# Kernel tuning notes

Hardware: AMD Instinct MI355X
Metric: run time of the kernel (lower is better)

Reference implementation:

```python
import jax, jax.numpy as jnp
import numpy as np

B, S, H = 4, 2048, 1024
DECAY_RATE = 0.5  # MemoryModule decay: exp(-decay_rate * k), k=1 (most recent pattern)


def setup_inputs() -> dict:
    key = jax.random.key(0)
    ks = jax.random.split(key, 7)
    hidden_states = jax.random.normal(ks[0], (B, S, H), dtype=jnp.float32)
    # past attention pattern: valid row-stochastic attention probs [B, S, S]
    pa = jax.random.uniform(ks[1], (B, S, S), dtype=jnp.float32)
    past_attention = pa / pa.sum(-1, keepdims=True)
    scale = 1.0 / np.sqrt(H).astype(np.float32)
    Wq = jax.random.normal(ks[2], (H, H), dtype=jnp.float32) * scale
    Wk = jax.random.normal(ks[3], (H, H), dtype=jnp.float32) * scale
    Wv = jax.random.normal(ks[4], (H, H), dtype=jnp.float32) * scale
    Wm = jax.random.normal(ks[5], (H, H), dtype=jnp.float32) * scale
    w_gate = jax.random.normal(ks[6], (H,), dtype=jnp.float32) * scale
    return {"hidden_states": hidden_states, "past_attention": past_attention,
            "Wq": Wq, "Wk": Wk, "Wv": Wv, "Wm": Wm, "w_gate": w_gate}


def reference(hidden_states, past_attention, Wq, Wk, Wv, Wm, w_gate):
    h = hidden_states.shape[-1]
    inv_sqrt_h = 1.0 / (h ** 0.5)
    # QKV projections (hidden -> hidden)
    q = jnp.einsum('bsh,hd->bsd', hidden_states, Wq)
    k = jnp.einsum('bsh,hd->bsd', hidden_states, Wk)
    v = jnp.einsum('bsh,hd->bsd', hidden_states, Wv)
    # base attention scores QK^T / sqrt(H)
    scores = jnp.einsum('bqd,bkd->bqk', q, k) * inv_sqrt_h
    # --- memory bias ---
    # decayed history pattern (single most-recent entry, k=1)
    memory = past_attention * jnp.exp(jnp.float32(-DECAY_RATE * 1.0))  # [B,S,S]
    # per-token scalar gate from query
    gates = jax.nn.sigmoid(jnp.einsum('bsh,h->bs', q, w_gate))  # [B,S]
    memory_values = jnp.einsum('bqk,bkd->bqd', memory, v)        # memory @ V
    transformed = jnp.einsum('bsh,hd->bsd', memory_values, Wm)   # memory_transform (no bias)
    gated_memory = gates[..., None] * transformed
    memory_bias = jnp.einsum('bqd,bkd->bqk', gated_memory, k) * inv_sqrt_h
    # augmented attention
    probs = jax.nn.softmax(scores + memory_bias, axis=-1)
    context = jnp.einsum('bqk,bkd->bqd', probs, v)
    return context
```

## Files before the change

kernel.cpp:

```cpp
#include <hip/hip_runtime.h>
#include <hip/hip_bf16.h>

typedef __attribute__((ext_vector_type(4))) float f32x4;
typedef __attribute__((ext_vector_type(8))) __bf16 bf16x8;

__device__ __forceinline__ unsigned short f2bf(float f) {
    union { float f; unsigned u; } x; x.f = f;
    unsigned r = x.u + 0x7fffu + ((x.u >> 16) & 1u);
    return (unsigned short)(r >> 16);
}
__device__ __forceinline__ float bf2f(unsigned short b) {
    union { unsigned u; float f; } x; x.u = ((unsigned)b) << 16;
    return x.f;
}

__device__ __forceinline__ void gload16(const void* g, void* l) {
    __builtin_amdgcn_global_load_lds(
        (const __attribute__((address_space(1))) unsigned int*)g,
        (__attribute__((address_space(3))) unsigned int*)l,
        16, 0, 0);
}

template <int N> __device__ __forceinline__ void vm_wait();
template <> __device__ __forceinline__ void vm_wait<0>() { asm volatile("s_waitcnt vmcnt(0)" ::: "memory"); }
template <> __device__ __forceinline__ void vm_wait<2>() { asm volatile("s_waitcnt vmcnt(2)" ::: "memory"); }
template <> __device__ __forceinline__ void vm_wait<4>() { asm volatile("s_waitcnt vmcnt(4)" ::: "memory"); }

__global__ __launch_bounds__(256) void k_prep(
    const float* __restrict__ hs, const float* __restrict__ pa,
    const float* __restrict__ Wq, const float* __restrict__ Wk,
    const float* __restrict__ Wv, const float* __restrict__ Wm,
    unsigned short* __restrict__ hs_bf, unsigned short* __restrict__ pa_bf,
    unsigned short* __restrict__ WT, float decay) {
    __shared__ float tile[32][33];
    unsigned b = blockIdx.x;
    int t = threadIdx.x;
    if (b < 16384u) {
        int i = b * 256 + t;
        float4 v = reinterpret_cast<const float4*>(pa)[i];
        union { unsigned short u[4]; uint2 q; } o;
        o.u[0] = f2bf(v.x * decay); o.u[1] = f2bf(v.y * decay);
        o.u[2] = f2bf(v.z * decay); o.u[3] = f2bf(v.w * decay);
        reinterpret_cast<uint2*>(pa_bf)[i] = o.q;
    } else if (b < 24576u) {
        int i = (b - 16384u) * 256 + t;
        float4 v = reinterpret_cast<const float4*>(hs)[i];
        union { unsigned short u[4]; uint2 q; } o;
        o.u[0] = f2bf(v.x); o.u[1] = f2bf(v.y);
        o.u[2] = f2bf(v.z); o.u[3] = f2bf(v.w);
        reinterpret_cast<uint2*>(hs_bf)[i] = o.q;
    } else {
        unsigned bb = b - 24576u;
        int z = bb >> 10, rem = bb & 1023;
        int bx = rem & 31, by = rem >> 5;
        const float* src = z == 0 ? Wq : z == 1 ? Wk : z == 2 ? Wv : Wm;
        unsigned short* dst = WT + (size_t)z * 1024 * 1024;
        int lx = t & 31, ly8 = t >> 5;
        int x = bx * 32 + lx;
#pragma unroll
        for (int i = 0; i < 4; i++)
            tile[ly8 + i * 8][lx] = src[(size_t)(by * 32 + ly8 + i * 8) * 1024 + x];
        __syncthreads();
        int tx = by * 32 + lx;
#pragma unroll
        for (int i = 0; i < 4; i++)
            dst[(size_t)(bx * 32 + ly8 + i * 8) * 1024 + tx] = f2bf(tile[lx][ly8 + i * 8]);
    }
}

__global__ __launch_bounds__(256) void k_post(
    const unsigned short* __restrict__ C3, unsigned short* __restrict__ v_t,
    const float* __restrict__ wg, float* __restrict__ gates) {
    __shared__ unsigned short tile[32][33];
    unsigned b = blockIdx.x;
    int t = threadIdx.x;
    if (b < 8192u) {
        int bx = b & 31, by = (b >> 5) & 63, bz = b >> 11;
        int lx = t & 31, ly8 = t >> 5;
        int x = bx * 32 + lx;
#pragma unroll
        for (int i = 0; i < 4; i++) {
            int y = by * 32 + ly8 + i * 8;
            tile[ly8 + i * 8][lx] = C3[(size_t)(bz * 2048 + y) * 3072 + 2048 + x];
        }
        __syncthreads();
        int tx = by * 32 + lx;
#pragma unroll
        for (int i = 0; i < 4; i++) {
            int ty = bx * 32 + ly8 + i * 8;
            v_t[(size_t)bz * 1024 * 2048 + (size_t)ty * 2048 + tx] = tile[lx][ly8 + i * 8];
        }
    } else {
        unsigned bb = b - 8192u;
        int lane = t & 63;
        int row = bb * 4 + (t >> 6);
        const unsigned short* qr = C3 + (size_t)row * 3072 + lane * 16;
        uint4 a0 = *reinterpret_cast<const uint4*>(qr);
        uint4 a1 = *reinterpret_cast<const uint4*>(qr + 8);
        const float* wp = wg + lane * 16;
        float s = 0.f;
        unsigned ua[8] = {a0.x, a0.y, a0.z, a0.w, a1.x, a1.y, a1.z, a1.w};
#pragma unroll
        for (int j = 0; j < 8; j++) {
            s += bf2f((unsigned short)(ua[j] & 0xffff)) * wp[2 * j];
            s += bf2f((unsigned short)(ua[j] >> 16)) * wp[2 * j + 1];
        }
#pragma unroll
        for (int o = 1; o < 64; o <<= 1) s += __shfl_xor(s, o);
        if (lane == 0) gates[row] = 1.f / (1.f + __expf(-s));
    }
}

__global__ __launch_bounds__(256) void k_inv(const float* __restrict__ partials,
                                             float* __restrict__ inv_s) {
    int r = blockIdx.x * 256 + threadIdx.x;
    const float4* p = reinterpret_cast<const float4*>(partials + (size_t)r * 8);
    float4 a = p[0], b = p[1];
    inv_s[r] = 1.f / (a.x + a.y + a.z + a.w + b.x + b.y + b.z + b.w);
}

template <int BN>
struct Geo {
    static constexpr int WN = BN / 64;
    static constexpr int WM = 8 / WN;
    static constexpr int WROWS = 256 / WM;
    static constexpr int MF = WROWS / 16;
    static constexpr int MP = MF / 4;
    static constexpr int ASZ = 256 * 64 * 2;
    static constexpr int BSZ = BN * 64 * 2;
    static constexpr int BUFSZ = ASZ + BSZ;
};

#define GPH(BUFOFF, MB, LB, STG, VMW)                                                   \
    {                                                                                   \
        const char* aB = smem + (BUFOFF);                                               \
        const char* bB = aB + G::ASZ;                                                   \
        bf16x8 af[G::MP * 2];                                                           \
        _Pragma("unroll") for (int mm = 0; mm < G::MP; ++mm)                            \
        _Pragma("unroll") for (int kk = 0; kk < 2; ++kk) {                              \
            int rowx = wrow + ((MB) + mm) * 16 + fr;                                    \
            int slot = (kk * 4 + kq) ^ (rowx & 7);                                      \
            af[mm * 2 + kk] = *reinterpret_cast<const bf16x8*>(aB + rowx * 128 + slot * 16); \
        }                                                                               \
        if (LB) {                                                                       \
            _Pragma("unroll") for (int nn = 0; nn < 4; ++nn)                            \
            _Pragma("unroll") for (int kk = 0; kk < 2; ++kk) {                          \
                int rowx = wcol + nn * 16 + fr;                                         \
                int slot = (kk * 4 + kq) ^ (rowx & 7);                                  \
                bfrag[nn * 2 + kk] = *reinterpret_cast<const bf16x8*>(bB + rowx * 128 + slot * 16); \
            }                                                                           \
        }                                                                               \
        STG;                                                                            \
        __builtin_amdgcn_sched_barrier(0);                                              \
        VMW;                                                                            \
        __builtin_amdgcn_s_barrier();                                                   \
        asm volatile("s_waitcnt lgkmcnt(0)" ::: "memory");                              \
        __builtin_amdgcn_sched_barrier(0);                                              \
        __builtin_amdgcn_s_setprio(1);                                                  \
        _Pragma("unroll") for (int mm = 0; mm < G::MP; ++mm)                            \
        _Pragma("unroll") for (int nn = 0; nn < 4; ++nn)                                \
        _Pragma("unroll") for (int kk = 0; kk < 2; ++kk)                                \
            acc[(MB) + mm][nn] = __builtin_amdgcn_mfma_f32_16x16x32_bf16(               \
                af[mm * 2 + kk], bfrag[nn * 2 + kk], acc[(MB) + mm][nn], 0, 0, 0);      \
        __builtin_amdgcn_s_setprio(0);                                                  \
        __builtin_amdgcn_sched_barrier(0);                                              \
        __builtin_amdgcn_s_barrier();                                                   \
        __builtin_amdgcn_sched_barrier(0);                                              \
    }

template <int EPI, int BN>
__global__ __launch_bounds__(512, 2) void k_gemm8(
    const unsigned short* __restrict__ A, int ldA, long long bsA,
    const unsigned short* __restrict__ Bt, int ldB, long long bsB,
    void* __restrict__ Cv, int ldC, long long bsC,
    const unsigned short* __restrict__ Qm, int ldQ,
    const float* __restrict__ gates, float alpha, int K,
    int NX, int NY, int NB, int yf) {
    using G = Geo<BN>;
    extern __shared__ char smem[];
    const int NT = K >> 6, NI = K >> 7;

    unsigned b = blockIdx.x;
    unsigned wg = (b & 7) * (gridDim.x >> 3) + (b >> 3);
    int xT, yT, zB;
    if (yf) {
        yT = wg % NY; unsigned r2 = wg / NY;
        xT = r2 % NX; zB = (int)(r2 / NX) % NB;
    } else {
        xT = wg % NX; unsigned r2 = wg / NX;
        yT = r2 % NY; zB = (int)(r2 / NY) % NB;
    }

    const unsigned short* Ab = A + (size_t)zB * (size_t)bsA;
    const unsigned short* Bb = Bt + (size_t)zB * (size_t)bsB;

    int t = threadIdx.x, lane = t & 63, wave = t >> 6;
    int wc = wave % G::WN, wr = wave / G::WN;
    int fr = lane & 15, kq = lane >> 4;
    int wrow = wr * G::WROWS, wcol = wc * 64;
    int trow = t >> 3, csx = (t & 7) ^ (trow & 7);
    long long rowTile = (long long)yT * 256, colTile = (long long)xT * BN;

    f32x4 acc[G::MF][4];
#pragma unroll
    for (int m = 0; m < G::MF; ++m)
#pragma unroll
        for (int n = 0; n < 4; ++n) acc[m][n] = (f32x4){0.f, 0.f, 0.f, 0.f};
    bf16x8 bfrag[8];

    auto stageA = [&](int buf, int h, int tt) {
        int kt = tt < NT ? tt : NT - 1;
#pragma unroll
        for (int rr = 0; rr < 2; ++rr) {
            const unsigned short* src =
                Ab + (size_t)(rowTile + h * 128 + rr * 64 + trow) * (size_t)ldA + kt * 64 + csx * 8;
            gload16(src, smem + buf * G::BUFSZ + h * 16384 + rr * 8192 + t * 16);
        }
    };
    auto stageB = [&](int buf, int h, int tt) {
        int kt = tt < NT ? tt : NT - 1;
        if (BN == 256) {
#pragma unroll
            for (int rr = 0; rr < 2; ++rr) {
                const unsigned short* src =
                    Bb + (size_t)(colTile + h * 128 + rr * 64 + trow) * (size_t)ldB + kt * 64 + csx * 8;
                gload16(src, smem + buf * G::BUFSZ + G::ASZ + h * 16384 + rr * 8192 + t * 16);
            }
        } else {
            const unsigned short* src =
                Bb + (size_t)(colTile + h * 64 + trow) * (size_t)ldB + kt * 64 + csx * 8;
            gload16(src, smem + buf * G::BUFSZ + G::ASZ + h * 8192 + t * 16);
        }
    };

    stageA(0, 0, 0); stageA(0, 1, 0);
    stageB(0, 0, 0); stageB(0, 1, 0);
    stageB(1, 0, 1); stageB(1, 1, 1);
    __builtin_amdgcn_sched_barrier(0);
    vm_wait<0>();
    __builtin_amdgcn_s_barrier();
    __builtin_amdgcn_sched_barrier(0);

    constexpr int VMN = (BN == 256) ? 4 : 2;
    for (int i = 0; i < NI; ++i) {
        int t1 = 2 * i + 1, t2 = 2 * i + 2, t3 = 2 * i + 3;
        GPH(0,          0,         1, stageA(1, 0, t1), (void)0);
        GPH(0,          G::MP,     0, stageA(1, 1, t1), (void)0);
        GPH(0,          2 * G::MP, 0, stageB(0, 0, t2), (void)0);
        GPH(0,          3 * G::MP, 0, stageB(0, 1, t2), vm_wait<VMN>());
        GPH(G::BUFSZ,   0,         1, stageA(0, 0, t2), (void)0);
        GPH(G::BUFSZ,   G::MP,     0, stageA(0, 1, t2), (void)0);
        GPH(G::BUFSZ,   2 * G::MP, 0, stageB(1, 0, t3), (void)0);
        GPH(G::BUFSZ,   3 * G::MP, 0, stageB(1, 1, t3), vm_wait<VMN>());
    }
    vm_wait<0>();

    long long rb0 = rowTile + wrow + kq * 4;
    long long cb0 = colTile + wcol + fr;
    if (EPI == 0) {
        unsigned short* C = (unsigned short*)Cv + (size_t)zB * (size_t)bsC;
#pragma unroll
        for (int m = 0; m < G::MF; ++m)
#pragma unroll
            for (int n = 0; n < 4; ++n)
#pragma unroll
                for (int r = 0; r < 4; ++r)
                    C[(size_t)(rb0 + m * 16 + r) * (size_t)ldC + cb0 + n * 16] =
                        f2bf(acc[m][n][r] * alpha);
    } else if (EPI == 1) {
        unsigned short* C = (unsigned short*)Cv;
#pragma unroll
        for (int m = 0; m < G::MF; ++m)
#pragma unroll
            for (int r = 0; r < 4; ++r) {
                long long row = rb0 + m * 16 + r;
                float g = gates[row];
#pragma unroll
                for (int n = 0; n < 4; ++n) {
                    long long col = cb0 + n * 16;
                    float v = (bf2f(Qm[(size_t)row * (size_t)ldQ + col]) + g * acc[m][n][r]) * alpha;
                    C[(size_t)row * (size_t)ldC + col] = f2bf(v);
                }
            }
    } else if (EPI == 4) {
        float* C = (float*)Cv + (size_t)zB * (size_t)bsC;
#pragma unroll
        for (int m = 0; m < G::MF; ++m)
#pragma unroll
            for (int r = 0; r < 4; ++r) {
                long long row = rb0 + m * 16 + r;
                float g = gates[(size_t)zB * (size_t)ldQ + row];
#pragma unroll
                for (int n = 0; n < 4; ++n)
                    C[(size_t)row * (size_t)ldC + cb0 + n * 16] = acc[m][n][r] * g;
            }
    } else if (EPI == 5) {
        unsigned short* C = (unsigned short*)Cv + (size_t)zB * (size_t)bsC;
        float* partials = (float*)gates;
        float srow[G::MF][4];
#pragma unroll
        for (int m = 0; m < G::MF; ++m)
#pragma unroll
            for (int r = 0; r < 4; ++r) srow[m][r] = 0.f;
#pragma unroll
        for (int m = 0; m < G::MF; ++m)
#pragma unroll
            for (int n = 0; n < 4; ++n)
#pragma unroll
                for (int r = 0; r < 4; ++r) {
                    float e = __expf(acc[m][n][r] * alpha);
                    C[(size_t)(rb0 + m * 16 + r) * (size_t)ldC + cb0 + n * 16] = f2bf(e);
                    srow[m][r] += e;
                }
#pragma unroll
        for (int m = 0; m < G::MF; ++m)
#pragma unroll
            for (int r = 0; r < 4; ++r) {
#pragma unroll
                for (int msk = 1; msk < 16; msk <<= 1)
                    srow[m][r] += __shfl_xor(srow[m][r], msk);
            }
        float* sums = (float*)smem;
        if (fr == 0) {
#pragma unroll
            for (int m = 0; m < G::MF; ++m)
#pragma unroll
                for (int r = 0; r < 4; ++r)
                    sums[(wrow + kq * 4 + m * 16 + r) * G::WN + wc] = srow[m][r];
        }
        __syncthreads();
        if (t < 256) {
            float s = 0.f;
#pragma unroll
            for (int j = 0; j < G::WN; ++j) s += sums[t * G::WN + j];
            partials[((size_t)zB * 2048 + (size_t)rowTile + t) * 8 + xT] = s;
        }
    }
}

extern "C" void kernel_launch(void* const* d_in, const int* in_sizes, int n_in,
                              void* d_out, int out_size, void* d_ws, size_t ws_size,
                              hipStream_t stream) {
    const float* hs = (const float*)d_in[0];
    const float* pa = (const float*)d_in[1];
    const float* Wq = (const float*)d_in[2];
    const float* Wk = (const float*)d_in[3];
    const float* Wv = (const float*)d_in[4];
    const float* Wm = (const float*)d_in[5];
    const float* wg = (const float*)d_in[6];
    float* out = (float*)d_out;

    const int B = 4, S = 2048, H = 1024;
    const size_t BS = (size_t)B * S;
    const size_t BSH = BS * H;
    const size_t BSS = (size_t)B * S * S;
    const float inv_sqrt_h = 0.03125f;
    const float decay = 0.60653065971263342f;

    char* ws = (char*)d_ws;
    size_t off = 0;
    auto take = [&](size_t bytes) {
        char* p = ws + off;
        off += (bytes + 255) & ~(size_t)255;
        return p;
    };
    unsigned short* hs_bf = (unsigned short*)take(BSH * 2);
    unsigned short* WT    = (unsigned short*)take(4ull * H * H * 2);
    float* gates          = (float*)take(BS * 4);
    unsigned short* C3    = (unsigned short*)take(BS * 3 * H * 2);
    unsigned short* v_t   = (unsigned short*)take(BSH * 2);
    unsigned short* pa_bf = (unsigned short*)take(BSS * 2);
    float* partials       = (float*)take(BS * 8 * 4);
    float* inv_s          = (float*)take(BS * 4);
    unsigned short* mv    = (unsigned short*)d_out;
    unsigned short* u_bf  = hs_bf;
    unsigned short* probs = pa_bf;
    unsigned short* WmT   = WT + 3ull * H * H;

    (void)hipFuncSetAttribute((const void*)k_gemm8<0, 128>, hipFuncAttributeMaxDynamicSharedMemorySize, 98304);
    (void)hipFuncSetAttribute((const void*)k_gemm8<1, 128>, hipFuncAttributeMaxDynamicSharedMemorySize, 98304);
    (void)hipFuncSetAttribute((const void*)k_gemm8<4, 128>, hipFuncAttributeMaxDynamicSharedMemorySize, 98304);
    (void)hipFuncSetAttribute((const void*)k_gemm8<5, 256>, hipFuncAttributeMaxDynamicSharedMemorySize, 131072);

    k_prep<<<dim3(28672), 256, 0, stream>>>(hs, pa, Wq, Wk, Wv, Wm, hs_bf, pa_bf, WT, decay);
    k_gemm8<0, 128><<<768, 512, 98304, stream>>>(
        hs_bf, H, 0, WT, H, 0, C3, 3 * H, 0, nullptr, 0, nullptr, 1.f, H, 24, 32, 1, 0);
    k_post<<<dim3(10240), 256, 0, stream>>>(C3, v_t, wg, gates);
    k_gemm8<0, 128><<<256, 512, 98304, stream>>>(
        pa_bf, S, (long long)S * S, v_t, S, (long long)H * S, mv, H, (long long)S * H,
        nullptr, 0, nullptr, 1.f, S, 8, 8, 4, 1);
    k_gemm8<1, 128><<<256, 512, 98304, stream>>>(
        mv, H, 0, WmT, H, 0, u_bf, H, 0, C3, 3 * H, gates, inv_sqrt_h, H, 8, 32, 1, 0);
    k_gemm8<5, 256><<<256, 512, 131072, stream>>>(
        u_bf, H, (long long)S * H, C3 + H, 3 * H, (long long)S * 3 * H,
        probs, S, (long long)S * S, nullptr, 0, partials, 1.f, H, 8, 8, 4, 1);
    k_inv<<<dim3(32), 256, 0, stream>>>(partials, inv_s);
    k_gemm8<4, 128><<<256, 512, 98304, stream>>>(
        probs, S, (long long)S * S, v_t, S, (long long)H * S, out, H, (long long)S * H,
        nullptr, S, inv_s, 1.f, S, 8, 8, 4, 1);
}
```

Baseline: 251.4 us.

## Fold gate projection into Wq·w_gate, fuse softmax normalization into ctx epilogue

Precomputes wg2 = Wq·w_gate so each token's gate becomes a dot product of hidden_states with wg2, evaluated in fp32 inside the hs conversion pass rather than as a separate read of the bf16 q. The k_inv launch goes away because the ctx GEMM epilogue now sums the 8 partial row sums and inverts them itself. The GEMM template is also split into distinctly named kernels, and the qkv and u launches switch their yf raster flag to 1. This cuts kernel launches and memory passes at the cost of a small extra kernel and redundant reciprocal work per epilogue row.

Result: slower. 259.0 us (+3.0%).

```diff
diff --git a/kernel.cpp b/kernel.cpp
--- a/kernel.cpp
+++ b/kernel.cpp
@@ -26,13 +26,32 @@
 template <> __device__ __forceinline__ void vm_wait<2>() { asm volatile("s_waitcnt vmcnt(2)" ::: "memory"); }
 template <> __device__ __forceinline__ void vm_wait<4>() { asm volatile("s_waitcnt vmcnt(4)" ::: "memory"); }
 
+__global__ __launch_bounds__(256) void k_wg2(const float* __restrict__ Wq,
+                                             const float* __restrict__ wg,
+                                             float* __restrict__ wg2) {
+    int lane = threadIdx.x & 63;
+    int row = blockIdx.x * 4 + (threadIdx.x >> 6);
+    const float4* a = reinterpret_cast<const float4*>(Wq + (size_t)row * 1024);
+    const float4* x = reinterpret_cast<const float4*>(wg);
+    float s = 0.f;
+    for (int i = lane; i < 256; i += 64) {
+        float4 av = a[i], bv = x[i];
+        s += av.x * bv.x + av.y * bv.y + av.z * bv.z + av.w * bv.w;
+    }
+#pragma unroll
+    for (int o = 1; o < 64; o <<= 1) s += __shfl_xor(s, o);
+    if (lane == 0) wg2[row] = s;
+}
+
 __global__ __launch_bounds__(256) void k_prep(
     const float* __restrict__ hs, const float* __restrict__ pa,
     const float* __restrict__ Wq, const float* __restrict__ Wk,
     const float* __restrict__ Wv, const float* __restrict__ Wm,
     unsigned short* __restrict__ hs_bf, unsigned short* __restrict__ pa_bf,
-    unsigned short* __restrict__ WT, float decay) {
+    unsigned short* __restrict__ WT, float decay,
+    const float* __restrict__ wg2, float* __restrict__ gates) {
     __shared__ float tile[32][33];
+    __shared__ float red[4];
     unsigned b = blockIdx.x;
     int t = threadIdx.x;
     if (b < 16384u) {
@@ -43,12 +62,23 @@
         o.u[2] = f2bf(v.z * decay); o.u[3] = f2bf(v.w * decay);
         reinterpret_cast<uint2*>(pa_bf)[i] = o.q;
     } else if (b < 24576u) {
-        int i = (b - 16384u) * 256 + t;
+        unsigned row = b - 16384u;
+        int i = row * 256 + t;
         float4 v = reinterpret_cast<const float4*>(hs)[i];
         union { unsigned short u[4]; uint2 q; } o;
         o.u[0] = f2bf(v.x); o.u[1] = f2bf(v.y);
         o.u[2] = f2bf(v.z); o.u[3] = f2bf(v.w);
         reinterpret_cast<uint2*>(hs_bf)[i] = o.q;
+        float4 w = reinterpret_cast<const float4*>(wg2)[t];
+        float s = v.x * w.x + v.y * w.y + v.z * w.z + v.w * w.w;
+#pragma unroll
+        for (int o2 = 1; o2 < 64; o2 <<= 1) s += __shfl_xor(s, o2);
+        if ((t & 63) == 0) red[t >> 6] = s;
+        __syncthreads();
+        if (t == 0) {
+            float ss = red[0] + red[1] + red[2] + red[3];
+            gates[row] = 1.f / (1.f + __expf(-ss));
+        }
     } else {
         unsigned bb = b - 24576u;
         int z = bb >> 10, rem = bb & 1023;
@@ -68,55 +98,26 @@
     }
 }
 
-__global__ __launch_bounds__(256) void k_post(
-    const unsigned short* __restrict__ C3, unsigned short* __restrict__ v_t,
-    const float* __restrict__ wg, float* __restrict__ gates) {
+__global__ __launch_bounds__(256) void k_post(const unsigned short* __restrict__ C3,
+                                              unsigned short* __restrict__ v_t) {
     __shared__ unsigned short tile[32][33];
     unsigned b = blockIdx.x;
     int t = threadIdx.x;
-    if (b < 8192u) {
-        int bx = b & 31, by = (b >> 5) & 63, bz = b >> 11;
-        int lx = t & 31, ly8 = t >> 5;
-        int x = bx * 32 + lx;
-#pragma unroll
-        for (int i = 0; i < 4; i++) {
-            int y = by * 32 + ly8 + i * 8;
-            tile[ly8 + i * 8][lx] = C3[(size_t)(bz * 2048 + y) * 3072 + 2048 + x];
-        }
-        __syncthreads();
-        int tx = by * 32 + lx;
-#pragma unroll
-        for (int i = 0; i < 4; i++) {
-            int ty = bx * 32 + ly8 + i * 8;
-            v_t[(size_t)bz * 1024 * 2048 + (size_t)ty * 2048 + tx] = tile[lx][ly8 + i * 8];
-        }
-    } else {
-        unsigned bb = b - 8192u;
-        int lane = t & 63;
-        int row = bb * 4 + (t >> 6);
-        const unsigned short* qr = C3 + (size_t)row * 3072 + lane * 16;
-        uint4 a0 = *reinterpret_cast<const uint4*>(qr);
-        uint4 a1 = *reinterpret_cast<const uint4*>(qr + 8);
-        const float* wp = wg + lane * 16;
-        float s = 0.f;
-        unsigned ua[8] = {a0.x, a0.y, a0.z, a0.w, a1.x, a1.y, a1.z, a1.w};
-#pragma unroll
-        for (int j = 0; j < 8; j++) {
-            s += bf2f((unsigned short)(ua[j] & 0xffff)) * wp[2 * j];
-            s += bf2f((unsigned short)(ua[j] >> 16)) * wp[2 * j + 1];
-        }
-#pragma unroll
-        for (int o = 1; o < 64; o <<= 1) s += __shfl_xor(s, o);
-        if (lane == 0) gates[row] = 1.f / (1.f + __expf(-s));
-    }
-}
-
-__global__ __launch_bounds__(256) void k_inv(const float* __restrict__ partials,
-                                             float* __restrict__ inv_s) {
-    int r = blockIdx.x * 256 + threadIdx.x;
-    const float4* p = reinterpret_cast<const float4*>(partials + (size_t)r * 8);
-    float4 a = p[0], b = p[1];
-    inv_s[r] = 1.f / (a.x + a.y + a.z + a.w + b.x + b.y + b.z + b.w);
+    int bx = b & 31, by = (b >> 5) & 63, bz = b >> 11;
+    int lx = t & 31, ly8 = t >> 5;
+    int x = bx * 32 + lx;
+#pragma unroll
+    for (int i = 0; i < 4; i++) {
+        int y = by * 32 + ly8 + i * 8;
+        tile[ly8 + i * 8][lx] = C3[(size_t)(bz * 2048 + y) * 3072 + 2048 + x];
+    }
+    __syncthreads();
+    int tx = by * 32 + lx;
+#pragma unroll
+    for (int i = 0; i < 4; i++) {
+        int ty = bx * 32 + ly8 + i * 8;
+        v_t[(size_t)bz * 1024 * 2048 + (size_t)ty * 2048 + tx] = tile[lx][ly8 + i * 8];
+    }
 }
 
 template <int BN>
@@ -169,7 +170,8 @@
     }
 
 template <int EPI, int BN>
-__global__ __launch_bounds__(512, 2) void k_gemm8(
+__device__ __forceinline__ void gemm_body(
+    char* smem,
     const unsigned short* __restrict__ A, int ldA, long long bsA,
     const unsigned short* __restrict__ Bt, int ldB, long long bsB,
     void* __restrict__ Cv, int ldC, long long bsC,
@@ -177,7 +179,6 @@
     const float* __restrict__ gates, float alpha, int K,
     int NX, int NY, int NB, int yf) {
     using G = Geo<BN>;
-    extern __shared__ char smem[];
     const int NT = K >> 6, NI = K >> 7;
 
     unsigned b = blockIdx.x;
@@ -289,7 +290,10 @@
 #pragma unroll
             for (int r = 0; r < 4; ++r) {
                 long long row = rb0 + m * 16 + r;
-                float g = gates[(size_t)zB * (size_t)ldQ + row];
+                const float4* pp = reinterpret_cast<const float4*>(
+                    gates + ((size_t)zB * 2048 + row) * 8);
+                float4 p0 = pp[0], p1 = pp[1];
+                float g = 1.f / (p0.x + p0.y + p0.z + p0.w + p1.x + p1.y + p1.z + p1.w);
 #pragma unroll
                 for (int n = 0; n < 4; ++n)
                     C[(size_t)row * (size_t)ldC + cb0 + n * 16] = acc[m][n][r] * g;
@@ -336,6 +340,34 @@
             partials[((size_t)zB * 2048 + (size_t)rowTile + t) * 8 + xT] = s;
         }
     }
+}
+
+#define GEMM_ARGS                                                                     \
+    const unsigned short *A, int ldA, long long bsA, const unsigned short *Bt,        \
+        int ldB, long long bsB, void *Cv, int ldC, long long bsC,                     \
+        const unsigned short *Qm, int ldQ, const float *gates, float alpha, int K,    \
+        int NX, int NY, int NB, int yf
+#define GEMM_PASS A, ldA, bsA, Bt, ldB, bsB, Cv, ldC, bsC, Qm, ldQ, gates, alpha, K, NX, NY, NB, yf
+
+__global__ __launch_bounds__(512, 2) void k_qkv(GEMM_ARGS) {
+    extern __shared__ char smem[];
+    gemm_body<0, 128>(smem, GEMM_PASS);
+}
+__global__ __launch_bounds__(512, 2) void k_mv(GEMM_ARGS) {
+    extern __shared__ char smem[];
+    gemm_body<0, 128>(smem, GEMM_PASS);
+}
+__global__ __launch_bounds__(512, 2) void k_u(GEMM_ARGS) {
+    extern __shared__ char smem[];
+    gemm_body<1, 128>(smem, GEMM_PASS);
+}
+__global__ __launch_bounds__(512, 2) void k_logits(GEMM_ARGS) {
+    extern __shared__ char smem[];
+    gemm_body<5, 256>(smem, GEMM_PASS);
+}
+__global__ __launch_bounds__(512, 2) void k_ctx(GEMM_ARGS) {
+    extern __shared__ char smem[];
+    gemm_body<4, 128>(smem, GEMM_PASS);
 }
 
 extern "C" void kernel_launch(void* const* d_in, const int* in_sizes, int n_in,
@@ -366,36 +398,37 @@
     };
     unsigned short* hs_bf = (unsigned short*)take(BSH * 2);
     unsigned short* WT    = (unsigned short*)take(4ull * H * H * 2);
+    float* wg2            = (float*)take(H * 4);
     float* gates          = (float*)take(BS * 4);
     unsigned short* C3    = (unsigned short*)take(BS * 3 * H * 2);
     unsigned short* v_t   = (unsigned short*)take(BSH * 2);
     unsigned short* pa_bf = (unsigned short*)take(BSS * 2);
     float* partials       = (float*)take(BS * 8 * 4);
-    float* inv_s          = (float*)take(BS * 4);
     unsigned short* mv    = (unsigned short*)d_out;
     unsigned short* u_bf  = hs_bf;
     unsigned short* probs = pa_bf;
     unsigned short* WmT   = WT + 3ull * H * H;
 
-    (void)hipFuncSetAttribute((const void*)k_gemm8<0, 128>, hipFuncAttributeMaxDynamicSharedMemorySize, 98304);
-    (void)hipFuncSetAttribute((const void*)k_gemm8<1, 128>, hipFuncAttributeMaxDynamicSharedMemorySize, 98304);
-    (void)hipFuncSetAttribute((const void*)k_gemm8<4, 128>, hipFuncAttributeMaxDynamicSharedMemorySize, 98304);
-    (void)hipFuncSetAttribute((const void*)k_gemm8<5, 256>, hipFuncAttributeMaxDynamicSharedMemorySize, 131072);
-
-    k_prep<<<dim3(28672), 256, 0, stream>>>(hs, pa, Wq, Wk, Wv, Wm, hs_bf, pa_bf, WT, decay);
-    k_gemm8<0, 128><<<768, 512, 98304, stream>>>(
-        hs_bf, H, 0, WT, H, 0, C3, 3 * H, 0, nullptr, 0, nullptr, 1.f, H, 24, 32, 1, 0);
-    k_post<<<dim3(10240), 256, 0, stream>>>(C3, v_t, wg, gates);
-    k_gemm8<0, 128><<<256, 512, 98304, stream>>>(
+    (void)hipFuncSetAttribute((const void*)k_qkv,    hipFuncAttributeMaxDynamicSharedMemorySize, 98304);
+    (void)hipFuncSetAttribute((const void*)k_mv,     hipFuncAttributeMaxDynamicSharedMemorySize, 98304);
+    (void)hipFuncSetAttribute((const void*)k_u,      hipFuncAttributeMaxDynamicSharedMemorySize, 98304);
+    (void)hipFuncSetAttribute((const void*)k_ctx,    hipFuncAttributeMaxDynamicSharedMemorySize, 98304);
+    (void)hipFuncSetAttribute((const void*)k_logits, hipFuncAttributeMaxDynamicSharedMemorySize, 131072);
+
+    k_wg2<<<dim3(256), 256, 0, stream>>>(Wq, wg, wg2);
+    k_prep<<<dim3(28672), 256, 0, stream>>>(hs, pa, Wq, Wk, Wv, Wm, hs_bf, pa_bf, WT, decay, wg2, gates);
+    k_qkv<<<768, 512, 98304, stream>>>(
+        hs_bf, H, 0, WT, H, 0, C3, 3 * H, 0, nullptr, 0, nullptr, 1.f, H, 24, 32, 1, 1);
+    k_post<<<dim3(8192), 256, 0, stream>>>(C3, v_t);
+    k_mv<<<256, 512, 98304, stream>>>(
         pa_bf, S, (long long)S * S, v_t, S, (long long)H * S, mv, H, (long long)S * H,
         nullptr, 0, nullptr, 1.f, S, 8, 8, 4, 1);
-    k_gemm8<1, 128><<<256, 512, 98304, stream>>>(
-        mv, H, 0, WmT, H, 0, u_bf, H, 0, C3, 3 * H, gates, inv_sqrt_h, H, 8, 32, 1, 0);
-    k_gemm8<5, 256><<<256, 512, 131072, stream>>>(
+    k_u<<<256, 512, 98304, stream>>>(
+        mv, H, 0, WmT, H, 0, u_bf, H, 0, C3, 3 * H, gates, inv_sqrt_h, H, 8, 32, 1, 1);
+    k_logits<<<256, 512, 131072, stream>>>(
         u_bf, H, (long long)S * H, C3 + H, 3 * H, (long long)S * 3 * H,
         probs, S, (long long)S * S, nullptr, 0, partials, 1.f, H, 8, 8, 4, 1);
-    k_inv<<<dim3(32), 256, 0, stream>>>(partials, inv_s);
-    k_gemm8<4, 128><<<256, 512, 98304, stream>>>(
+    k_ctx<<<256, 512, 98304, stream>>>(
         probs, S, (long long)S * S, v_t, S, (long long)H * S, out, H, (long long)S * H,
-        nullptr, S, inv_s, 1.f, S, 8, 8, 4, 1);
-}
+        nullptr, 0, partials, 1.f, S, 8, 8, 4, 1);
+}
```
